# Kernel optimization log

Measured on AMD Instinct MI355X. Metric: run time of the kernel, lower is better.

Reference implementation:

```python
import jax, jax.numpy as jnp
import numpy as np

NUM_DISPARITIES = 64


def setup_inputs() -> dict:
    key = jax.random.key(0)
    k1, k2 = jax.random.split(key)
    B, C, H, W = 4, 32, 256, 512
    left = jax.random.normal(k1, (B, C, H, W), dtype=jnp.float32)
    right = jax.random.normal(k2, (B, C, H, W), dtype=jnp.float32)
    return {"left": left, "right": right}


def cost_volume(left, right, num_disparities):
    # left, right: [B, C, H, W] -> output [B, D, H, W]
    W = left.shape[3]
    wcoord = jnp.arange(W)  # [W]

    def one_disparity(i):
        # right shifted so rs[..., w] == right[..., w - i] for w >= i
        rs = jnp.roll(right, i, axis=3)
        corr = jnp.mean(left * rs, axis=1)  # [B, H, W] channel-mean dot product
        # zero out invalid columns w < i (matches zeros-init + slice write in torch)
        return jnp.where(wcoord >= i, corr, jnp.zeros_like(corr))

    # sequential map over disparities keeps peak memory at one [B,C,H,W] product
    out = jax.lax.map(one_disparity, jnp.arange(num_disparities))  # [D, B, H, W]
    return jnp.transpose(out, (1, 0, 2, 3))  # [B, D, H, W]


def reference(left, right):
    return cost_volume(left, right, NUM_DISPARITIES)
```

## Files before the change

### kernel.cpp

```cpp
#include <hip/hip_runtime.h>


constexpr int Bn = 4, Cn = 32, Hn = 256, Wn = 512, Dn = 64;
constexpr int CCH = 8;
constexpr int WT = 4, DT = 16;
constexpr int PAD = 64;
constexpr int STRIDE = PAD + Wn;
constexpr int HW = Hn * Wn;
constexpr int RBUF = CCH * STRIDE;
constexpr int LBUF = CCH * Wn;

__global__ __launch_bounds__(512, 4)
void cost_volume_kernel(const float* __restrict__ left,
                        const float* __restrict__ right,
                        float* __restrict__ out)
{
    __shared__ __align__(16) float Rs[2][RBUF];
    __shared__ __align__(16) float Ls[2][LBUF];

    const int tid = threadIdx.x;
    const int bh  = blockIdx.x;
    const int b   = bh >> 8;
    const int h   = bh & (Hn - 1);

    const float* Lrow = left  + (b * Cn * Hn + h) * Wn;
    const float* Rrow = right + (b * Cn * Hn + h) * Wn;

    if (tid < 2 * CCH * (PAD / 4)) {
        const int s  = tid >> 7;
        const int c  = (tid >> 4) & (CCH - 1);
        const int wq = (tid & 15) << 2;
        *reinterpret_cast<float4*>(&Rs[s][c * STRIDE + wq]) =
            make_float4(0.f, 0.f, 0.f, 0.f);
    }

    auto stage = [&](int sel, int cc) {
        #pragma unroll
        for (int k = 0; k < 2; ++k) {
            const int f = tid + (k << 9);
            const int c = f >> 7;
            const int w = (f & 127) << 2;
            __builtin_amdgcn_global_load_lds(
                (const __attribute__((address_space(1))) void*)(Rrow + (cc + c) * HW + w),
                (__attribute__((address_space(3))) void*)(&Rs[sel][c * STRIDE + PAD + w]),
                16, 0, 0);
            __builtin_amdgcn_global_load_lds(
                (const __attribute__((address_space(1))) void*)(Lrow + (cc + c) * HW + w),
                (__attribute__((address_space(3))) void*)(&Ls[sel][c * Wn + w]),
                16, 0, 0);
        }
    };

    const int tw = tid & 127;
    const int td = tid >> 7;
    const int w0 = tw << 2;
    const int d0 = td << 4;
    const int rbase = PAD + w0 - d0 - 16;

    float acc[DT][WT];
    #pragma unroll
    for (int j = 0; j < DT; ++j)
        #pragma unroll
        for (int i = 0; i < WT; ++i)
            acc[j][i] = 0.f;

    stage(0, 0);

    int sel = 0;
    for (int cc = 0; cc < Cn; cc += CCH) {
        __syncthreads();

        if (cc + CCH < Cn)
            stage(sel ^ 1, cc + CCH);

        const float* Rb = &Rs[sel][0];
        const float* Lb = &Ls[sel][0];

        #pragma unroll 2
        for (int c = 0; c < CCH; ++c) {
            const float4 Lv =
                *reinterpret_cast<const float4*>(&Lb[c * Wn + w0]);

            const float* rp = &Rb[c * STRIDE + rbase];
            float r[20];
            #pragma unroll
            for (int q = 0; q < 5; ++q)
                *reinterpret_cast<float4*>(&r[q * 4]) =
                    *reinterpret_cast<const float4*>(&rp[q * 4]);

            #pragma unroll
            for (int j = 0; j < DT; ++j) {
                acc[j][0] = fmaf(Lv.x, r[16 - j], acc[j][0]);
                acc[j][1] = fmaf(Lv.y, r[17 - j], acc[j][1]);
                acc[j][2] = fmaf(Lv.z, r[18 - j], acc[j][2]);
                acc[j][3] = fmaf(Lv.w, r[19 - j], acc[j][3]);
            }
        }
        sel ^= 1;
    }

    constexpr float inv = 1.0f / 32.0f;
    float* op = out + ((b * Dn + d0) * Hn + h) * Wn + w0;
    #pragma unroll
    for (int j = 0; j < DT; ++j) {
        const float4 v = make_float4(acc[j][0] * inv, acc[j][1] * inv,
                                     acc[j][2] * inv, acc[j][3] * inv);
        *reinterpret_cast<float4*>(&op[j * HW]) = v;
    }
}

extern "C" void kernel_launch(void* const* d_in, const int* in_sizes, int n_in,
                              void* d_out, int out_size, void* d_ws, size_t ws_size,
                              hipStream_t stream) {
    const float* left  = (const float*)d_in[0];
    const float* right = (const float*)d_in[1];
    float* out = (float*)d_out;
    cost_volume_kernel<<<dim3(Bn * Hn), dim3(512), 0, stream>>>(left, right, out);
}
```

Baseline: 244.9 us.

## Deepen LDS staging to four-buffer pipeline with explicit vmcnt waits

Switches from a double-buffered 8-channel staging loop to a four-buffer ring of 4-channel chunks, issuing three chunks ahead and fully unrolling the channel-chunk loop. Explicit s_waitcnt vmcnt counts plus raw s_barrier replace __syncthreads, so each step waits only for the chunk it is about to consume. The aim is more global-to-LDS loads in flight while FMAs run. LDS use stays about the same, but the hand-written vmcnt values depend on the exact number of outstanding loads per thread, which is fragile.

```diff
diff --git a/kernel.cpp b/kernel.cpp
--- a/kernel.cpp
+++ b/kernel.cpp
@@ -2,7 +2,9 @@
 
 
 constexpr int Bn = 4, Cn = 32, Hn = 256, Wn = 512, Dn = 64;
-constexpr int CCH = 8;
+constexpr int CCH = 4;
+constexpr int NCHUNK = Cn / CCH;
+constexpr int NBUF = 4;
 constexpr int WT = 4, DT = 16;
 constexpr int PAD = 64;
 constexpr int STRIDE = PAD + Wn;
@@ -15,8 +17,8 @@
                         const float* __restrict__ right,
                         float* __restrict__ out)
 {
-    __shared__ __align__(16) float Rs[2][RBUF];
-    __shared__ __align__(16) float Ls[2][LBUF];
+    __shared__ __align__(16) float Rs[NBUF * RBUF];
+    __shared__ __align__(16) float Ls[NBUF * LBUF];
 
     const int tid = threadIdx.x;
     const int bh  = blockIdx.x;
@@ -26,30 +28,33 @@
     const float* Lrow = left  + (b * Cn * Hn + h) * Wn;
     const float* Rrow = right + (b * Cn * Hn + h) * Wn;
 
-    if (tid < 2 * CCH * (PAD / 4)) {
-        const int s  = tid >> 7;
-        const int c  = (tid >> 4) & (CCH - 1);
-        const int wq = (tid & 15) << 2;
-        *reinterpret_cast<float4*>(&Rs[s][c * STRIDE + wq]) =
+    if (tid < NBUF * CCH * (PAD / 4)) {
+        const int buf = tid >> 6;
+        const int c   = (tid >> 4) & (CCH - 1);
+        const int wq  = (tid & 15) << 2;
+        *reinterpret_cast<float4*>(&Rs[buf * RBUF + c * STRIDE + wq]) =
             make_float4(0.f, 0.f, 0.f, 0.f);
     }
 
-    auto stage = [&](int sel, int cc) {
-        #pragma unroll
-        for (int k = 0; k < 2; ++k) {
-            const int f = tid + (k << 9);
-            const int c = f >> 7;
-            const int w = (f & 127) << 2;
-            __builtin_amdgcn_global_load_lds(
-                (const __attribute__((address_space(1))) void*)(Rrow + (cc + c) * HW + w),
-                (__attribute__((address_space(3))) void*)(&Rs[sel][c * STRIDE + PAD + w]),
-                16, 0, 0);
-            __builtin_amdgcn_global_load_lds(
-                (const __attribute__((address_space(1))) void*)(Lrow + (cc + c) * HW + w),
-                (__attribute__((address_space(3))) void*)(&Ls[sel][c * Wn + w]),
-                16, 0, 0);
-        }
+    const int sc = tid >> 7;
+    const int sw = (tid & 127) << 2;
+    auto stage = [&](int sel, int chunk) {
+        const int gc = chunk * CCH + sc;
+        __builtin_amdgcn_global_load_lds(
+            (const __attribute__((address_space(1))) void*)(Rrow + gc * HW + sw),
+            (__attribute__((address_space(3))) void*)(&Rs[sel * RBUF + sc * STRIDE + PAD + sw]),
+            16, 0, 0);
+        __builtin_amdgcn_global_load_lds(
+            (const __attribute__((address_space(1))) void*)(Lrow + gc * HW + sw),
+            (__attribute__((address_space(3))) void*)(&Ls[sel * LBUF + sc * Wn + sw]),
+            16, 0, 0);
     };
+
+    __syncthreads();
+
+    stage(0, 0);
+    stage(1, 1);
+    stage(2, 2);
 
     const int tw = tid & 127;
     const int td = tid >> 7;
@@ -64,17 +69,20 @@
         for (int i = 0; i < WT; ++i)
             acc[j][i] = 0.f;
 
-    stage(0, 0);
+    #pragma unroll
+    for (int t = 0; t < NCHUNK; ++t) {
+        if (t < 6)       asm volatile("s_waitcnt vmcnt(4)" ::: "memory");
+        else if (t == 6) asm volatile("s_waitcnt vmcnt(2)" ::: "memory");
+        else             asm volatile("s_waitcnt vmcnt(0)" ::: "memory");
+        __builtin_amdgcn_sched_barrier(0);
+        __builtin_amdgcn_s_barrier();
+        __builtin_amdgcn_sched_barrier(0);
 
-    int sel = 0;
-    for (int cc = 0; cc < Cn; cc += CCH) {
-        __syncthreads();
+        if (t + 3 < NCHUNK)
+            stage((t + 3) & (NBUF - 1), t + 3);
 
-        if (cc + CCH < Cn)
-            stage(sel ^ 1, cc + CCH);
-
-        const float* Rb = &Rs[sel][0];
-        const float* Lb = &Ls[sel][0];
+        const float* Rb = &Rs[(t & (NBUF - 1)) * RBUF];
+        const float* Lb = &Ls[(t & (NBUF - 1)) * LBUF];
 
         #pragma unroll 2
         for (int c = 0; c < CCH; ++c) {
@@ -96,7 +104,6 @@
                 acc[j][3] = fmaf(Lv.w, r[19 - j], acc[j][3]);
             }
         }
-        sel ^= 1;
     }
 
     constexpr float inv = 1.0f / 32.0f;
```

Result: slower. 254.7 us (+4.0%).
